# Kernel tuning notes

Measured on AMD Instinct MI355X. Metric: run time of the kernel, lower is better.

## Reference

```python
import jax, jax.numpy as jnp
import numpy as np
import math

NQ = 6        # n_qubits_data
NL = 2        # n_layers (active_layers == n_layers)
K = 3         # unfold kernel
C = 64        # channels
SD = 128      # style_dim
B, H, W = 8, 64, 64
PD = C * K * K  # patch_dim = 576


def _apply_1q(psi, U, w):
    # psi: [bsz, 2,2,...,2]; U: [2,2] or [bsz,2,2]
    psi = jnp.moveaxis(psi, 1 + w, -1)
    if U.ndim == 2:
        psi = jnp.einsum('...j,ij->...i', psi, U)
    else:
        psi = jnp.einsum('b...j,bij->b...i', psi, U)
    return jnp.moveaxis(psi, -1, 1 + w)


def _ry_mat(theta):
    c = jnp.cos(theta / 2)
    s = jnp.sin(theta / 2)
    m = jnp.stack([jnp.stack([c, -s], -1), jnp.stack([s, c], -1)], -2)
    return m.astype(jnp.complex64)


def _rz_mat(theta):
    t = theta.astype(jnp.complex64)
    em = jnp.exp(-0.5j * t)
    ep = jnp.exp(0.5j * t)
    z = jnp.zeros_like(em)
    return jnp.stack([jnp.stack([em, z], -1), jnp.stack([z, ep], -1)], -2)


def _u3_mat(theta, phi, lam):
    t = theta.astype(jnp.complex64)
    p = phi.astype(jnp.complex64)
    l = lam.astype(jnp.complex64)
    ct = jnp.cos(t / 2)
    st = jnp.sin(t / 2)
    return jnp.stack([
        jnp.stack([ct, -jnp.exp(1j * l) * st], -1),
        jnp.stack([jnp.exp(1j * p) * st, jnp.exp(1j * (p + l)) * ct], -1)
    ], -2)


def _cnot(psi, c, t):
    c0, c1 = jnp.split(psi, 2, axis=1 + c)
    c1 = jnp.flip(c1, axis=1 + t)
    return jnp.concatenate([c0, c1], axis=1 + c)


def _forward(x, style, data_proj_w, data_proj_b, style_to_data_w, style_to_data_b,
             qcnn_rot_params, measure_params, out_proj_w, out_proj_b,
             res_proj_w, res_proj_b):
    Bx, Cx, Hx, Wx = x.shape
    # nn.Unfold(3, padding=1): [B, C*9, H*W], channel-major then kernel pos
    xp = jnp.pad(x, ((0, 0), (0, 0), (1, 1), (1, 1)))
    pats = jnp.stack([xp[:, :, i:i + Hx, j:j + Wx]
                      for i in range(K) for j in range(K)], axis=2)  # [B,C,9,H,W]
    patches_flat = pats.reshape(Bx, Cx * K * K, Hx * Wx).transpose(0, 2, 1).reshape(-1, Cx * K * K)
    style_flat = jnp.broadcast_to(style[:, None, :], (Bx, Hx * Wx, style.shape[-1])).reshape(-1, style.shape[-1])

    data_angles = jnp.tanh(patches_flat @ data_proj_w.T + data_proj_b) * math.pi   # [bsz, NQ]
    style_angles = jnp.tanh(style_flat @ style_to_data_w.T + style_to_data_b) * math.pi

    bsz = patches_flat.shape[0]
    psi = jnp.zeros((bsz,) + (2,) * NQ, jnp.complex64)
    psi = psi.at[(slice(None),) + (0,) * NQ].set(1.0)

    # hybrid encoding: RY(data + style) per wire (batched angles)
    theta0 = data_angles + style_angles
    for i in range(NQ):
        psi = _apply_1q(psi, _ry_mat(theta0[:, i]), i)

    # HEA layers: per-wire RY/RZ (scalar params) + ring CNOTs
    for l in range(NL):
        for i in range(NQ):
            psi = _apply_1q(psi, _ry_mat(qcnn_rot_params[l, i, 0, 0]), i)
            psi = _apply_1q(psi, _rz_mat(qcnn_rot_params[l, i, 1, 0]), i)
        for i in range(NQ):
            psi = _cnot(psi, i, (i + 1) % NQ)

    # trainable measurement basis (U3 per wire)
    for i in range(NQ):
        psi = _apply_1q(psi, _u3_mat(measure_params[i, 0], measure_params[i, 1], measure_params[i, 2]), i)

    # PauliZ expvals on all wires
    probs = psi.real ** 2 + psi.imag ** 2
    expvals = []
    for i in range(NQ):
        p = jnp.sum(probs, axis=tuple(a for a in range(1, NQ + 1) if a != 1 + i))  # [bsz,2]
        expvals.append(p[:, 0] - p[:, 1])
    quant_out = jnp.stack(expvals, -1)  # [bsz, NQ]

    out_flat = (quant_out @ out_proj_w.T + out_proj_b) + (patches_flat @ res_proj_w.T + res_proj_b)
    return out_flat.reshape(Bx, Hx, Wx, -1).transpose(0, 3, 1, 2)


def setup_inputs() -> dict:
    key = jax.random.key(0)
    ks = jax.random.split(key, 10)
    return {
        'x': jax.random.normal(ks[0], (B, C, H, W), jnp.float32),
        'style': jax.random.normal(ks[1], (B, SD), jnp.float32),
        'data_proj_w': jax.random.normal(ks[2], (NQ, PD), jnp.float32) * 0.02,
        'data_proj_b': jnp.zeros((NQ,), jnp.float32),
        'style_to_data_w': jax.random.normal(ks[3], (NQ, SD), jnp.float32) * 0.02,
        'style_to_data_b': jnp.zeros((NQ,), jnp.float32),
        'qcnn_rot_params': jax.random.normal(ks[4], (NL, NQ, 2, 3), jnp.float32) * 0.1,
        'measure_params': jax.random.normal(ks[5], (NQ, 3), jnp.float32) * 0.1,
        'out_proj_w': jax.random.normal(ks[6], (C, NQ), jnp.float32) * 0.02,
        'out_proj_b': jnp.zeros((C,), jnp.float32),
        'res_proj_w': jax.random.normal(ks[7], (C, PD), jnp.float32) * 0.02,
        'res_proj_b': jnp.zeros((C,), jnp.float32),
    }


def reference(x, style, data_proj_w, data_proj_b, style_to_data_w, style_to_data_b,
              qcnn_rot_params, measure_params, out_proj_w, out_proj_b,
              res_proj_w, res_proj_b):
    return _forward(x, style, data_proj_w, data_proj_b, style_to_data_w, style_to_data_b,
                    qcnn_rot_params, measure_params, out_proj_w, out_proj_b,
                    res_proj_w, res_proj_b)
```

## Files before the change

### kernel.cpp

```cpp
#include <hip/hip_runtime.h>
#include <math.h>

#define PI_F 3.14159265358979323846f

typedef __attribute__((ext_vector_type(8))) short bf16x8;
typedef __attribute__((ext_vector_type(4))) float f32x4;

__device__ float g_sang[48];
__device__ float g_cb[64];
__device__ __attribute__((aligned(16))) unsigned short g_Urb[64 * 64];
__device__ __attribute__((aligned(16))) unsigned short g_Uib[64 * 64];
__device__ __attribute__((aligned(16))) unsigned short g_Zwc[64 * 64];
__device__ __attribute__((aligned(16))) unsigned short g_Bm[5 * 18 * 64 * 8];

__device__ inline unsigned short bf16rne(float f) {
    unsigned u = __float_as_uint(f);
    return (unsigned short)((u + 0x7FFFu + ((u >> 16) & 1u)) >> 16);
}
__device__ inline float rlane(float v, int k) {
    return __uint_as_float(__builtin_amdgcn_readlane(__float_as_uint(v), k));
}

__global__ __launch_bounds__(1024) void k_prep(
        const float* __restrict__ style,
        const float* __restrict__ dw, const float* __restrict__ rw,
        const float* __restrict__ s2dw, const float* __restrict__ s2db,
        const float* __restrict__ qcnn, const float* __restrict__ meas,
        const float* __restrict__ outw, const float* __restrict__ outb,
        const float* __restrict__ resb) {
    int bid  = blockIdx.x;
    int tid  = threadIdx.x;
    int lane = tid & 63;
    int wid  = tid >> 6;

    if (bid >= 1 && bid <= 6) {
        int entry = (bid - 1) * 1024 + tid;
        if (entry < 5760) {
            int nt   = entry / 1152;
            int rem  = entry - nt * 1152;
            int slab = rem >> 6;
            int ln   = rem & 63;
            int mm   = ln & 15, qq = ln >> 4;
            int n    = nt * 16 + mm;
            int ij   = slab >> 1;
            int ch   = (slab & 1) * 32 + qq * 8;
            unsigned pk[4] = {0u, 0u, 0u, 0u};
            if (n < 70) {
                const float* src = (n < 64) ? (rw + n * 576 + ij)
                                            : (dw + (n - 64) * 576 + ij);
#pragma unroll
                for (int jj = 0; jj < 4; ++jj) {
                    pk[jj] = (unsigned)bf16rne(src[(ch + 2 * jj) * 9])
                           | ((unsigned)bf16rne(src[(ch + 2 * jj + 1) * 9]) << 16);
                }
            }
            *(uint4*)(g_Bm + entry * 8) = make_uint4(pk[0], pk[1], pk[2], pk[3]);
        }
        return;
    }

    if (bid == 7) {
        float zr[6];
#pragma unroll
        for (int q = 0; q < 6; ++q) zr[q] = ((lane >> (5 - q)) & 1) ? -1.f : 1.f;
#pragma unroll
        for (int cc = 0; cc < 4; ++cc) {
            int c = wid * 4 + cc;
            float z = 0.f;
#pragma unroll
            for (int q = 0; q < 6; ++q) z += outw[c * 6 + q] * zr[q];
            g_Zwc[c * 64 + lane] = bf16rne(z);
        }
        if (wid == 0) g_cb[lane] = outb[lane] + resb[lane];
        if (wid == 1 && lane < 48) {
            int bb = lane / 6, q = lane % 6;
            float a = s2db[q];
#pragma unroll 8
            for (int j = 0; j < 128; ++j) a += style[bb * 128 + j] * s2dw[q * 128 + j];
            g_sang[lane] = tanhf(a) * PI_F;
        }
        return;
    }

    float tsv, tcv;
    {
        int idx = lane < 48 ? lane : 0;
        float arg;
        if (idx < 24) {
            arg = 0.5f * qcnn[idx * 3];
        } else {
            int q3 = (idx - 24) >> 2, part = (idx - 24) & 3;
            float th = meas[q3 * 3 + 0], ph = meas[q3 * 3 + 1], lm = meas[q3 * 3 + 2];
            arg = part == 0 ? 0.5f * th : part == 1 ? lm : part == 2 ? ph : ph + lm;
        }
        sincosf(arg, &tsv, &tcv);
    }
    int s0 = wid * 4;
    float ar[4], ai[4];
#pragma unroll
    for (int cc = 0; cc < 4; ++cc) {
        ar[cc] = (lane == s0 + cc) ? 1.f : 0.f;
        ai[cc] = 0.f;
    }
#pragma unroll
    for (int l = 0; l < 2; ++l) {
#pragma unroll
        for (int wq = 0; wq < 6; ++wq) {
            int mask = 1 << (5 - wq);
            bool hi = (lane & mask) != 0;
            int g = (l * 6 + wq) * 2;
            float sg = rlane(tsv, g),     cg = rlane(tcv, g);
            float sz = rlane(tsv, g + 1), cz = rlane(tcv, g + 1);
            float szz = hi ? sz : -sz;
#pragma unroll
            for (int cc = 0; cc < 4; ++cc) {
                float pr  = __shfl_xor(ar[cc], mask);
                float pi2 = __shfl_xor(ai[cc], mask);
                float nr = hi ? (sg * pr + cg * ar[cc]) : (cg * ar[cc] - sg * pr);
                float ni = hi ? (sg * pi2 + cg * ai[cc]) : (cg * ai[cc] - sg * pi2);
                ar[cc] = cz * nr - szz * ni;
                ai[cc] = cz * ni + szz * nr;
            }
        }
#pragma unroll
        for (int wq = 0; wq < 6; ++wq) {
            int cm = 1 << (5 - wq);
            int tm = 1 << (5 - ((wq + 1) % 6));
#pragma unroll
            for (int cc = 0; cc < 4; ++cc) {
                float pr  = __shfl_xor(ar[cc], tm);
                float pi2 = __shfl_xor(ai[cc], tm);
                if (lane & cm) { ar[cc] = pr; ai[cc] = pi2; }
            }
        }
    }
#pragma unroll
    for (int wq = 0; wq < 6; ++wq) {
        int mask = 1 << (5 - wq);
        bool hi = (lane & mask) != 0;
        int u = 24 + wq * 4;
        float st2 = rlane(tsv, u),     ct  = rlane(tcv, u);
        float sl  = rlane(tsv, u + 1), cl  = rlane(tcv, u + 1);
        float sp  = rlane(tsv, u + 2), cp  = rlane(tcv, u + 2);
        float spl = rlane(tsv, u + 3), cpl = rlane(tcv, u + 3);
        float u01r = -cl * st2, u01i = -sl * st2;
        float u10r =  cp * st2, u10i =  sp * st2;
        float u11r =  cpl * ct, u11i =  spl * ct;
#pragma unroll
        for (int cc = 0; cc < 4; ++cc) {
            float pr  = __shfl_xor(ar[cc], mask);
            float pi2 = __shfl_xor(ai[cc], mask);
            float nr, ni;
            if (hi) {
                nr = u10r * pr - u10i * pi2 + u11r * ar[cc] - u11i * ai[cc];
                ni = u10r * pi2 + u10i * pr + u11r * ai[cc] + u11i * ar[cc];
            } else {
                nr = ct * ar[cc] + u01r * pr - u01i * pi2;
                ni = ct * ai[cc] + u01r * pi2 + u01i * pr;
            }
            ar[cc] = nr; ai[cc] = ni;
        }
    }
    unsigned short rr[4], ii[4];
#pragma unroll
    for (int cc = 0; cc < 4; ++cc) { rr[cc] = bf16rne(ar[cc]); ii[cc] = bf16rne(ai[cc]); }
    *(uint2*)(g_Urb + lane * 64 + s0) =
        make_uint2((unsigned)rr[0] | ((unsigned)rr[1] << 16),
                   (unsigned)rr[2] | ((unsigned)rr[3] << 16));
    *(uint2*)(g_Uib + lane * 64 + s0) =
        make_uint2((unsigned)ii[0] | ((unsigned)ii[1] << 16),
                   (unsigned)ii[2] | ((unsigned)ii[3] << 16));
}

__global__ __launch_bounds__(1024, 8) void k_main(const float* __restrict__ x,
                                                  const float* __restrict__ dpb,
                                                  float* __restrict__ out) {
    __shared__ __attribute__((aligned(16))) float smem[7640];
    unsigned*             xsu32 = (unsigned*)smem;
    const unsigned short* xsu   = (const unsigned short*)smem;
    float*          fact    = smem;
    unsigned short* psi_bf  = (unsigned short*)(smem + 1024);
    unsigned short* p_bf    = (unsigned short*)(smem + 3328);
    float*          angs    = smem + 7128;

    int tid  = threadIdx.x;
    int lane = tid & 63;
    int wid  = __builtin_amdgcn_readfirstlane(tid >> 6);
    int m    = lane & 15;
    int quad = lane >> 4;

    int p = blockIdx.x * 64 + lane;
    int b = p >> 12;
    int h = (p >> 6) & 63;
    const float* xb = x + (b << 18);

    if (tid < 216) {
        int r3 = tid / 72, rest = tid % 72;
        int half = rest / 36, cp = rest % 36;
        xsu32[(r3 * 66 + half * 65) * 36 + cp] = 0u;
    }
#pragma unroll
    for (int k = 0; k < 6; ++k) {
        int flat = k * 1024 + tid;
        int row  = flat >> 11;
        int rem  = flat & 2047;
        int cp   = rem >> 6;
        int w2   = rem & 63;
        int hh   = h + row - 1;
        float v0 = 0.f, v1 = 0.f;
        if ((unsigned)hh < 64u) {
            const float* px = xb + (hh << 6) + w2;
            v0 = px[(2 * cp) << 12];
            v1 = px[(2 * cp + 1) << 12];
        }
        xsu32[(row * 66 + w2 + 1) * 36 + cp] =
            (unsigned)bf16rne(v0) | ((unsigned)bf16rne(v1) << 16);
    }
    __syncthreads();

    int mt0 = wid >> 2, nt0 = wid & 3;
    const unsigned short* a0base = xsu + (mt0 * 16 + m) * 72 + quad * 8;
    const unsigned short* b0base = g_Bm + ((nt0 * 18) * 64 + lane) * 8;
    f32x4 acc0 = {0.f, 0.f, 0.f, 0.f};
    f32x4 acc1 = {0.f, 0.f, 0.f, 0.f};
    if (wid < 4) {
        const unsigned short* a1base = xsu + (wid * 16 + m) * 72 + quad * 8;
        const unsigned short* b1base = g_Bm + ((4 * 18) * 64 + lane) * 8;
#pragma unroll
        for (int slab = 0; slab < 18; ++slab) {
            int ij = slab >> 1, i = ij / 3, j = ij - 3 * (ij / 3);
            int aoff = i * 4752 + j * 72 + (slab & 1) * 32;
            bf16x8 a0 = *(const bf16x8*)(a0base + aoff);
            bf16x8 b0 = *(const bf16x8*)(b0base + slab * 512);
            acc0 = __builtin_amdgcn_mfma_f32_16x16x32_bf16(a0, b0, acc0, 0, 0, 0);
            bf16x8 a1 = *(const bf16x8*)(a1base + aoff);
            bf16x8 b1 = *(const bf16x8*)(b1base + slab * 512);
            acc1 = __builtin_amdgcn_mfma_f32_16x16x32_bf16(a1, b1, acc1, 0, 0, 0);
        }
    } else {
#pragma unroll
        for (int slab = 0; slab < 18; ++slab) {
            int ij = slab >> 1, i = ij / 3, j = ij - 3 * (ij / 3);
            int aoff = i * 4752 + j * 72 + (slab & 1) * 32;
            bf16x8 a0 = *(const bf16x8*)(a0base + aoff);
            bf16x8 b0 = *(const bf16x8*)(b0base + slab * 512);
            acc0 = __builtin_amdgcn_mfma_f32_16x16x32_bf16(a0, b0, acc0, 0, 0, 0);
        }
    }
    if (wid < 4 && m < 6) {
#pragma unroll
        for (int r = 0; r < 4; ++r) {
            angs[(wid * 16 + quad * 4 + r) * 8 + m] = acc1[r];
        }
    }
    __syncthreads();

    if (wid < 6) {
        int q = wid;
        float tv = angs[lane * 8 + q];
        float theta = tanhf(tv + dpb[q]) * PI_F + g_sang[b * 6 + q];
        float sv, cv; sincosf(0.5f * theta, &sv, &cv);
        fact[q * 64 + lane] = sv;
        fact[(6 + q) * 64 + lane] = cv;
    }
    __syncthreads();

    {
        float f0s = fact[0 * 64 + lane], f0c = fact[6 * 64 + lane];
        float f1s = fact[1 * 64 + lane], f1c = fact[7 * 64 + lane];
        float f2s = fact[2 * 64 + lane], f2c = fact[8 * 64 + lane];
        float f3s = fact[3 * 64 + lane], f3c = fact[9 * 64 + lane];
        float f4s = fact[4 * 64 + lane], f4c = fact[10 * 64 + lane];
        float f5s = fact[5 * 64 + lane], f5c = fact[11 * 64 + lane];
        int sb = wid * 4;
        float pre = (((sb >> 5) & 1) ? f0s : f0c)
                  * (((sb >> 4) & 1) ? f1s : f1c)
                  * (((sb >> 3) & 1) ? f2s : f2c)
                  * (((sb >> 2) & 1) ? f3s : f3c);
        unsigned short pk[4];
#pragma unroll
        for (int ti = 0; ti < 4; ++ti) {
            float v = pre * ((ti & 2) ? f4s : f4c) * ((ti & 1) ? f5s : f5c);
            pk[ti] = bf16rne(v);
        }
        *(uint2*)(psi_bf + lane * 72 + sb) =
            make_uint2((unsigned)pk[0] | ((unsigned)pk[1] << 16),
                       (unsigned)pk[2] | ((unsigned)pk[3] << 16));
    }
    __syncthreads();

    {
        const unsigned short* pa = psi_bf + (mt0 * 16 + m) * 72 + quad * 8;
        const unsigned short* ur = g_Urb + (nt0 * 16 + m) * 64 + quad * 8;
        const unsigned short* ui = g_Uib + (nt0 * 16 + m) * 64 + quad * 8;
        bf16x8 aA = *(const bf16x8*)(pa);
        bf16x8 aB = *(const bf16x8*)(pa + 32);
        f32x4 c1 = {0.f, 0.f, 0.f, 0.f};
        f32x4 c2 = {0.f, 0.f, 0.f, 0.f};
        c1 = __builtin_amdgcn_mfma_f32_16x16x32_bf16(aA, *(const bf16x8*)(ur), c1, 0, 0, 0);
        c1 = __builtin_amdgcn_mfma_f32_16x16x32_bf16(aB, *(const bf16x8*)(ur + 32), c1, 0, 0, 0);
        c2 = __builtin_amdgcn_mfma_f32_16x16x32_bf16(aA, *(const bf16x8*)(ui), c2, 0, 0, 0);
        c2 = __builtin_amdgcn_mfma_f32_16x16x32_bf16(aB, *(const bf16x8*)(ui + 32), c2, 0, 0, 0);
#pragma unroll
        for (int r = 0; r < 4; ++r) {
            float pv = c1[r] * c1[r] + c2[r] * c2[r];
            p_bf[(mt0 * 16 + quad * 4 + r) * 72 + nt0 * 16 + m] = bf16rne(pv);
        }
    }
    __syncthreads();

    {
        const unsigned short* pa = p_bf + (mt0 * 16 + m) * 72 + quad * 8;
        const unsigned short* zc = g_Zwc + (nt0 * 16 + m) * 64 + quad * 8;
        f32x4 o = {0.f, 0.f, 0.f, 0.f};
        o = __builtin_amdgcn_mfma_f32_16x16x32_bf16(*(const bf16x8*)(pa),
                                                    *(const bf16x8*)(zc), o, 0, 0, 0);
        o = __builtin_amdgcn_mfma_f32_16x16x32_bf16(*(const bf16x8*)(pa + 32),
                                                    *(const bf16x8*)(zc + 32), o, 0, 0, 0);
        int cch = nt0 * 16 + m;
        float cbv = g_cb[cch];
        float4 res;
        res.x = (acc0[0] + o[0]) + cbv;
        res.y = (acc0[1] + o[1]) + cbv;
        res.z = (acc0[2] + o[2]) + cbv;
        res.w = (acc0[3] + o[3]) + cbv;
        int base = (b << 18) + (cch << 12) + (h << 6) + mt0 * 16 + quad * 4;
        *(float4*)(out + base) = res;
    }
}

extern "C" void kernel_launch(void* const* d_in, const int* in_sizes, int n_in,
                              void* d_out, int out_size, void* d_ws, size_t ws_size,
                              hipStream_t stream) {
    const float* x     = (const float*)d_in[0];
    const float* style = (const float*)d_in[1];
    const float* dw    = (const float*)d_in[2];
    const float* dpb   = (const float*)d_in[3];
    const float* s2dw  = (const float*)d_in[4];
    const float* s2db  = (const float*)d_in[5];
    const float* qcnn  = (const float*)d_in[6];
    const float* meas  = (const float*)d_in[7];
    const float* outw  = (const float*)d_in[8];
    const float* outb  = (const float*)d_in[9];
    const float* rw    = (const float*)d_in[10];
    const float* resb  = (const float*)d_in[11];
    float* out = (float*)d_out;

    hipLaunchKernelGGL(k_prep, dim3(8), dim3(1024), 0, stream,
                       style, dw, rw, s2dw, s2db, qcnn, meas, outw, outb, resb);
    hipLaunchKernelGGL(k_main, dim3(512), dim3(1024), 0, stream, x, dpb, out);
}
```

Baseline: 110.3 us.

## Halve k_main block size, give each wave two M-tiles, and pad LDS stride

Shrinks the main kernel from 1024 to 512 threads per block. Each of the 8 waves now computes two 16-row M-tiles, so every B fragment (conv weights, U matrices, measurement weights) loaded from global memory is reused across two MFMAs. The LDS row stride of the staged input goes from 36 to 37 dwords (72 to 74 bf16), which is meant to reduce LDS bank conflicts on the A-fragment reads. In exchange each wave carries more work and more accumulators, and there are fewer waves per block to hide latency.

```diff
diff --git a/kernel.cpp b/kernel.cpp
--- a/kernel.cpp
+++ b/kernel.cpp
@@ -172,16 +172,16 @@
                    (unsigned)ii[2] | ((unsigned)ii[3] << 16));
 }
 
-__global__ __launch_bounds__(1024, 8) void k_main(const float* __restrict__ x,
-                                                  const float* __restrict__ dpb,
-                                                  float* __restrict__ out) {
-    __shared__ __attribute__((aligned(16))) float smem[7640];
+__global__ __launch_bounds__(512, 8) void k_main(const float* __restrict__ x,
+                                                 const float* __restrict__ dpb,
+                                                 float* __restrict__ out) {
+    __shared__ __attribute__((aligned(16))) float smem[7838];
     unsigned*             xsu32 = (unsigned*)smem;
     const unsigned short* xsu   = (const unsigned short*)smem;
     float*          fact    = smem;
     unsigned short* psi_bf  = (unsigned short*)(smem + 1024);
     unsigned short* p_bf    = (unsigned short*)(smem + 3328);
-    float*          angs    = smem + 7128;
+    float*          angs    = smem + 7326;
 
     int tid  = threadIdx.x;
     int lane = tid & 63;
@@ -194,14 +194,14 @@
     int h = (p >> 6) & 63;
     const float* xb = x + (b << 18);
 
-    if (tid < 216) {
-        int r3 = tid / 72, rest = tid % 72;
-        int half = rest / 36, cp = rest % 36;
-        xsu32[(r3 * 66 + half * 65) * 36 + cp] = 0u;
-    }
-#pragma unroll
-    for (int k = 0; k < 6; ++k) {
-        int flat = k * 1024 + tid;
+    if (tid < 222) {
+        int r3 = tid / 74, rest = tid % 74;
+        int half = rest / 37, cp = rest % 37;
+        xsu32[(r3 * 66 + half * 65) * 37 + cp] = 0u;
+    }
+#pragma unroll
+    for (int k = 0; k < 12; ++k) {
+        int flat = k * 512 + tid;
         int row  = flat >> 11;
         int rem  = flat & 2047;
         int cp   = rem >> 6;
@@ -213,26 +213,31 @@
             v0 = px[(2 * cp) << 12];
             v1 = px[(2 * cp + 1) << 12];
         }
-        xsu32[(row * 66 + w2 + 1) * 36 + cp] =
+        xsu32[(row * 66 + w2 + 1) * 37 + cp] =
             (unsigned)bf16rne(v0) | ((unsigned)bf16rne(v1) << 16);
     }
     __syncthreads();
 
-    int mt0 = wid >> 2, nt0 = wid & 3;
-    const unsigned short* a0base = xsu + (mt0 * 16 + m) * 72 + quad * 8;
+    int mtA = wid >> 2;
+    int nt0 = wid & 3;
+    const unsigned short* aAbase = xsu + (mtA * 16 + m) * 74 + quad * 8;
+    const unsigned short* aBbase = xsu + ((mtA + 2) * 16 + m) * 74 + quad * 8;
     const unsigned short* b0base = g_Bm + ((nt0 * 18) * 64 + lane) * 8;
-    f32x4 acc0 = {0.f, 0.f, 0.f, 0.f};
-    f32x4 acc1 = {0.f, 0.f, 0.f, 0.f};
+    f32x4 acc0a = {0.f, 0.f, 0.f, 0.f};
+    f32x4 acc0b = {0.f, 0.f, 0.f, 0.f};
+    f32x4 acc1  = {0.f, 0.f, 0.f, 0.f};
     if (wid < 4) {
-        const unsigned short* a1base = xsu + (wid * 16 + m) * 72 + quad * 8;
+        const unsigned short* a1base = xsu + (wid * 16 + m) * 74 + quad * 8;
         const unsigned short* b1base = g_Bm + ((4 * 18) * 64 + lane) * 8;
 #pragma unroll
         for (int slab = 0; slab < 18; ++slab) {
             int ij = slab >> 1, i = ij / 3, j = ij - 3 * (ij / 3);
-            int aoff = i * 4752 + j * 72 + (slab & 1) * 32;
-            bf16x8 a0 = *(const bf16x8*)(a0base + aoff);
+            int aoff = i * 4884 + j * 74 + (slab & 1) * 32;
             bf16x8 b0 = *(const bf16x8*)(b0base + slab * 512);
-            acc0 = __builtin_amdgcn_mfma_f32_16x16x32_bf16(a0, b0, acc0, 0, 0, 0);
+            bf16x8 aA = *(const bf16x8*)(aAbase + aoff);
+            acc0a = __builtin_amdgcn_mfma_f32_16x16x32_bf16(aA, b0, acc0a, 0, 0, 0);
+            bf16x8 aB = *(const bf16x8*)(aBbase + aoff);
+            acc0b = __builtin_amdgcn_mfma_f32_16x16x32_bf16(aB, b0, acc0b, 0, 0, 0);
             bf16x8 a1 = *(const bf16x8*)(a1base + aoff);
             bf16x8 b1 = *(const bf16x8*)(b1base + slab * 512);
             acc1 = __builtin_amdgcn_mfma_f32_16x16x32_bf16(a1, b1, acc1, 0, 0, 0);
@@ -241,10 +246,12 @@
 #pragma unroll
         for (int slab = 0; slab < 18; ++slab) {
             int ij = slab >> 1, i = ij / 3, j = ij - 3 * (ij / 3);
-            int aoff = i * 4752 + j * 72 + (slab & 1) * 32;
-            bf16x8 a0 = *(const bf16x8*)(a0base + aoff);
+            int aoff = i * 4884 + j * 74 + (slab & 1) * 32;
             bf16x8 b0 = *(const bf16x8*)(b0base + slab * 512);
-            acc0 = __builtin_amdgcn_mfma_f32_16x16x32_bf16(a0, b0, acc0, 0, 0, 0);
+            bf16x8 aA = *(const bf16x8*)(aAbase + aoff);
+            acc0a = __builtin_amdgcn_mfma_f32_16x16x32_bf16(aA, b0, acc0a, 0, 0, 0);
+            bf16x8 aB = *(const bf16x8*)(aBbase + aoff);
+            acc0b = __builtin_amdgcn_mfma_f32_16x16x32_bf16(aB, b0, acc0b, 0, 0, 0);
         }
     }
     if (wid < 4 && m < 6) {
@@ -272,60 +279,76 @@
         float f3s = fact[3 * 64 + lane], f3c = fact[9 * 64 + lane];
         float f4s = fact[4 * 64 + lane], f4c = fact[10 * 64 + lane];
         float f5s = fact[5 * 64 + lane], f5c = fact[11 * 64 + lane];
-        int sb = wid * 4;
+        int sb = wid * 8;
         float pre = (((sb >> 5) & 1) ? f0s : f0c)
                   * (((sb >> 4) & 1) ? f1s : f1c)
-                  * (((sb >> 3) & 1) ? f2s : f2c)
-                  * (((sb >> 2) & 1) ? f3s : f3c);
-        unsigned short pk[4];
-#pragma unroll
-        for (int ti = 0; ti < 4; ++ti) {
-            float v = pre * ((ti & 2) ? f4s : f4c) * ((ti & 1) ? f5s : f5c);
+                  * (((sb >> 3) & 1) ? f2s : f2c);
+        unsigned short pk[8];
+#pragma unroll
+        for (int ti = 0; ti < 8; ++ti) {
+            float v = pre * ((ti & 4) ? f3s : f3c)
+                          * ((ti & 2) ? f4s : f4c)
+                          * ((ti & 1) ? f5s : f5c);
             pk[ti] = bf16rne(v);
         }
-        *(uint2*)(psi_bf + lane * 72 + sb) =
-            make_uint2((unsigned)pk[0] | ((unsigned)pk[1] << 16),
-                       (unsigned)pk[2] | ((unsigned)pk[3] << 16));
+        *(uint4*)(psi_bf + lane * 72 + sb) =
+            make_uint4((unsigned)pk[0] | ((unsigned)pk[1] << 16),
+                       (unsigned)pk[2] | ((unsigned)pk[3] << 16),
+                       (unsigned)pk[4] | ((unsigned)pk[5] << 16),
+                       (unsigned)pk[6] | ((unsigned)pk[7] << 16));
     }
     __syncthreads();
 
     {
-        const unsigned short* pa = psi_bf + (mt0 * 16 + m) * 72 + quad * 8;
         const unsigned short* ur = g_Urb + (nt0 * 16 + m) * 64 + quad * 8;
         const unsigned short* ui = g_Uib + (nt0 * 16 + m) * 64 + quad * 8;
-        bf16x8 aA = *(const bf16x8*)(pa);
-        bf16x8 aB = *(const bf16x8*)(pa + 32);
-        f32x4 c1 = {0.f, 0.f, 0.f, 0.f};
-        f32x4 c2 = {0.f, 0.f, 0.f, 0.f};
-        c1 = __builtin_amdgcn_mfma_f32_16x16x32_bf16(aA, *(const bf16x8*)(ur), c1, 0, 0, 0);
-        c1 = __builtin_amdgcn_mfma_f32_16x16x32_bf16(aB, *(const bf16x8*)(ur + 32), c1, 0, 0, 0);
-        c2 = __builtin_amdgcn_mfma_f32_16x16x32_bf16(aA, *(const bf16x8*)(ui), c2, 0, 0, 0);
-        c2 = __builtin_amdgcn_mfma_f32_16x16x32_bf16(aB, *(const bf16x8*)(ui + 32), c2, 0, 0, 0);
-#pragma unroll
-        for (int r = 0; r < 4; ++r) {
-            float pv = c1[r] * c1[r] + c2[r] * c2[r];
-            p_bf[(mt0 * 16 + quad * 4 + r) * 72 + nt0 * 16 + m] = bf16rne(pv);
+        bf16x8 ur0 = *(const bf16x8*)(ur);
+        bf16x8 ur1 = *(const bf16x8*)(ur + 32);
+        bf16x8 ui0 = *(const bf16x8*)(ui);
+        bf16x8 ui1 = *(const bf16x8*)(ui + 32);
+#pragma unroll
+        for (int half = 0; half < 2; ++half) {
+            int mt = mtA + half * 2;
+            const unsigned short* pa = psi_bf + (mt * 16 + m) * 72 + quad * 8;
+            bf16x8 aA = *(const bf16x8*)(pa);
+            bf16x8 aB = *(const bf16x8*)(pa + 32);
+            f32x4 c1 = {0.f, 0.f, 0.f, 0.f};
+            f32x4 c2 = {0.f, 0.f, 0.f, 0.f};
+            c1 = __builtin_amdgcn_mfma_f32_16x16x32_bf16(aA, ur0, c1, 0, 0, 0);
+            c1 = __builtin_amdgcn_mfma_f32_16x16x32_bf16(aB, ur1, c1, 0, 0, 0);
+            c2 = __builtin_amdgcn_mfma_f32_16x16x32_bf16(aA, ui0, c2, 0, 0, 0);
+            c2 = __builtin_amdgcn_mfma_f32_16x16x32_bf16(aB, ui1, c2, 0, 0, 0);
+#pragma unroll
+            for (int r = 0; r < 4; ++r) {
+                float pv = c1[r] * c1[r] + c2[r] * c2[r];
+                p_bf[(mt * 16 + quad * 4 + r) * 72 + nt0 * 16 + m] = bf16rne(pv);
+            }
         }
     }
     __syncthreads();
 
     {
-        const unsigned short* pa = p_bf + (mt0 * 16 + m) * 72 + quad * 8;
         const unsigned short* zc = g_Zwc + (nt0 * 16 + m) * 64 + quad * 8;
-        f32x4 o = {0.f, 0.f, 0.f, 0.f};
-        o = __builtin_amdgcn_mfma_f32_16x16x32_bf16(*(const bf16x8*)(pa),
-                                                    *(const bf16x8*)(zc), o, 0, 0, 0);
-        o = __builtin_amdgcn_mfma_f32_16x16x32_bf16(*(const bf16x8*)(pa + 32),
-                                                    *(const bf16x8*)(zc + 32), o, 0, 0, 0);
+        bf16x8 zc0 = *(const bf16x8*)(zc);
+        bf16x8 zc1 = *(const bf16x8*)(zc + 32);
         int cch = nt0 * 16 + m;
         float cbv = g_cb[cch];
-        float4 res;
-        res.x = (acc0[0] + o[0]) + cbv;
-        res.y = (acc0[1] + o[1]) + cbv;
-        res.z = (acc0[2] + o[2]) + cbv;
-        res.w = (acc0[3] + o[3]) + cbv;
-        int base = (b << 18) + (cch << 12) + (h << 6) + mt0 * 16 + quad * 4;
-        *(float4*)(out + base) = res;
+#pragma unroll
+        for (int half = 0; half < 2; ++half) {
+            int mt = mtA + half * 2;
+            const unsigned short* pa = p_bf + (mt * 16 + m) * 72 + quad * 8;
+            f32x4 o = {0.f, 0.f, 0.f, 0.f};
+            o = __builtin_amdgcn_mfma_f32_16x16x32_bf16(*(const bf16x8*)(pa), zc0, o, 0, 0, 0);
+            o = __builtin_amdgcn_mfma_f32_16x16x32_bf16(*(const bf16x8*)(pa + 32), zc1, o, 0, 0, 0);
+            f32x4 acc = half ? acc0b : acc0a;
+            float4 res;
+            res.x = (acc[0] + o[0]) + cbv;
+            res.y = (acc[1] + o[1]) + cbv;
+            res.z = (acc[2] + o[2]) + cbv;
+            res.w = (acc[3] + o[3]) + cbv;
+            int base = (b << 18) + (cch << 12) + (h << 6) + mt * 16 + quad * 4;
+            *(float4*)(out + base) = res;
+        }
     }
 }
 
@@ -348,5 +371,5 @@
 
     hipLaunchKernelGGL(k_prep, dim3(8), dim3(1024), 0, stream,
                        style, dw, rw, s2dw, s2db, qcnn, meas, outw, outb, resb);
-    hipLaunchKernelGGL(k_main, dim3(512), dim3(1024), 0, stream, x, dpb, out);
-}
+    hipLaunchKernelGGL(k_main, dim3(512), dim3(512), 0, stream, x, dpb, out);
+}
```

New measurement: 122.7 us. 11.2% more time.
